# Kernel tuning notes

Hardware: AMD Instinct MI355X
Metric: run time of the kernel (lower is better)

The kernel has to match this reference:

```python
import jax, jax.numpy as jnp
import numpy as np

DIM = 512
GROUPS = 8

def setup_inputs() -> dict:
    key = jax.random.key(0)
    k1, k2, k3, k4, k5 = jax.random.split(key, 5)
    B, L, C = 8, 4096, DIM
    s = 1.0 / np.sqrt(C)
    x = jax.random.normal(k1, (B, L, C), dtype=jnp.float32)
    W_qkv = jax.random.normal(k2, (C, 3 * C), dtype=jnp.float32) * s
    b_qkv = jax.random.normal(k3, (3 * C,), dtype=jnp.float32) * 0.01
    W_proj = jax.random.normal(k4, (C, C), dtype=jnp.float32) * s
    b_proj = jax.random.normal(k5, (C,), dtype=jnp.float32) * 0.01
    return {"x": x, "W_qkv": W_qkv, "b_qkv": b_qkv,
            "W_proj": W_proj, "b_proj": b_proj, "size": 64}

def reference(x, W_qkv, b_qkv, W_proj, b_proj, size):
    B, L, C = x.shape
    g = GROUPS
    hd = C // g  # per-group channel dim
    qkv = x @ W_qkv + b_qkv                       # [B, L, 3C]
    qkv = qkv.reshape(B, L, 3, g, hd).transpose(2, 0, 3, 1, 4)  # [3, B, g, L, hd]
    q, k, v = qkv[0], qkv[1], qkv[2]
    q = q * (float(L) ** -0.5)
    # channel-wise (cross-covariance) attention: [B, g, hd, hd]
    attn = jnp.einsum('bgld,bgle->bgde', q, k)
    attn = jax.nn.softmax(attn, axis=-1)
    out = jnp.einsum('bgde,bgle->bgld', attn, v)  # [B, g, L, hd]
    out = out.transpose(0, 2, 1, 3).reshape(B, L, C)
    out = out @ W_proj + b_proj
    return (out, size)
```

## Files before the change

kernel.cpp:

```cpp
#include <hip/hip_runtime.h>
#include <hip/hip_bf16.h>
#include <stdint.h>

typedef __hip_bfloat16 bf16;
typedef __attribute__((ext_vector_type(8))) short s16x8;
typedef __attribute__((ext_vector_type(4))) float f32x4;

__device__ __forceinline__ short f2bf_bits(float f) {
    union { bf16 b; short s; } u; u.b = __float2bfloat16(f); return u.s;
}

__device__ __forceinline__ void gload_lds16(const void* g, void* l) {
    __builtin_amdgcn_global_load_lds(
        (const __attribute__((address_space(1))) void*)(uintptr_t)g,
        (__attribute__((address_space(3))) void*)(uintptr_t)l,
        16, 0, 0);
}

__device__ __forceinline__ f32x4 mfma16(s16x8 a, s16x8 b, f32x4 c) {
    return __builtin_amdgcn_mfma_f32_16x16x32_bf16(a, b, c, 0, 0, 0);
}

__global__ __launch_bounds__(256) void cvt_bf16_kernel(const float* __restrict__ in,
                                                       bf16* __restrict__ out, int n8) {
    int i = blockIdx.x * blockDim.x + threadIdx.x;
    int stride = gridDim.x * blockDim.x;
    for (; i < n8; i += stride) {
        f32x4 a = ((const f32x4*)in)[2 * i];
        f32x4 b = ((const f32x4*)in)[2 * i + 1];
        s16x8 o;
        o[0] = f2bf_bits(a[0]); o[1] = f2bf_bits(a[1]);
        o[2] = f2bf_bits(a[2]); o[3] = f2bf_bits(a[3]);
        o[4] = f2bf_bits(b[0]); o[5] = f2bf_bits(b[1]);
        o[6] = f2bf_bits(b[2]); o[7] = f2bf_bits(b[3]);
        ((s16x8*)out)[i] = o;
    }
}

__global__ __launch_bounds__(256) void transpose_cvt_kernel(const float* __restrict__ in,
                                                            bf16* __restrict__ out,
                                                            int R, int C) {
    __shared__ float t[32][33];
    int c0 = blockIdx.x * 32, r0 = blockIdx.y * 32;
    int lx = threadIdx.x & 31, ly = threadIdx.x >> 5;
    for (int i = ly; i < 32; i += 8)
        t[i][lx] = in[(size_t)(r0 + i) * C + (c0 + lx)];
    __syncthreads();
    for (int i = ly; i < 32; i += 8)
        out[(size_t)(c0 + i) * R + (r0 + lx)] = __float2bfloat16(t[lx][i]);
}

__global__ __launch_bounds__(256, 2) void gemm_qkv_kernel(
    const bf16* __restrict__ A, const bf16* __restrict__ Bt,
    const float* __restrict__ bias,
    bf16* __restrict__ qT, bf16* __restrict__ kT, bf16* __restrict__ V) {
    __shared__ __align__(16) char smem[33280];
    bf16* As = (bf16*)smem;
    bf16* Bs = (bf16*)(smem + 16384);
    const int tid = threadIdx.x;
    const int wid = tid >> 6, lane = tid & 63;
    const int r16 = lane & 15, rg = lane >> 4;
    const int wr = wid >> 1, wc = wid & 1;
    const int n0 = blockIdx.x * 128;
    const int m0 = blockIdx.y * 128;

    f32x4 acc[4][4] = {};
    for (int ks = 0; ks < 8; ++ks) {
        const int k0 = ks * 64;
#pragma unroll
        for (int it = 0; it < 4; ++it) {
            int f = (it * 256 + tid) << 4;
            int row = f >> 7;
            int sc = ((f >> 4) & 7) ^ (row & 7);
            gload_lds16((const char*)(A + (size_t)(m0 + row) * 512 + k0) + (sc << 4),
                        (char*)As + ((it * 256 + (wid << 6)) << 4));
            gload_lds16((const char*)(Bt + (size_t)(n0 + row) * 512 + k0) + (sc << 4),
                        (char*)Bs + ((it * 256 + (wid << 6)) << 4));
        }
        __syncthreads();
#pragma unroll
        for (int kk = 0; kk < 2; ++kk) {
            s16x8 af[4], bfv[4];
#pragma unroll
            for (int mi = 0; mi < 4; ++mi) {
                int row = (wr << 6) + (mi << 4) + r16;
                int off = (row << 7) + ((((kk << 2) + rg) ^ (row & 7)) << 4);
                af[mi] = *(const s16x8*)((const char*)As + off);
            }
#pragma unroll
            for (int ni = 0; ni < 4; ++ni) {
                int row = (wc << 6) + (ni << 4) + r16;
                int off = (row << 7) + ((((kk << 2) + rg) ^ (row & 7)) << 4);
                bfv[ni] = *(const s16x8*)((const char*)Bs + off);
            }
#pragma unroll
            for (int mi = 0; mi < 4; ++mi)
#pragma unroll
                for (int ni = 0; ni < 4; ++ni)
                    acc[mi][ni] = mfma16(af[mi], bfv[ni], acc[mi][ni]);
        }
        __syncthreads();
    }

    const int bb = m0 >> 12;
    const int l0 = m0 & 4095;
    const float scale = (n0 < 512) ? 0.015625f : 1.0f;
    bf16* tr = (bf16*)smem;
    float bv[4];
#pragma unroll
    for (int ni = 0; ni < 4; ++ni)
        bv[ni] = bias[n0 + (wc << 6) + (ni << 4) + r16];
#pragma unroll
    for (int mi = 0; mi < 4; ++mi)
#pragma unroll
        for (int ni = 0; ni < 4; ++ni) {
            int col = (wc << 6) + (ni << 4) + r16;
#pragma unroll
            for (int r = 0; r < 4; ++r) {
                int row = (wr << 6) + (mi << 4) + (rg << 2) + r;
                tr[row * 130 + col] = __float2bfloat16((acc[mi][ni][r] + bv[ni]) * scale);
            }
        }
    __syncthreads();
    if (n0 < 1024) {
        bf16* dst; int c0;
        if (n0 < 512) { dst = qT; c0 = n0; } else { dst = kT; c0 = n0 - 512; }
#pragma unroll 4
        for (int it = 0; it < 64; ++it) {
            int flat = it * 256 + tid;
            int cl = flat >> 7, ll = flat & 127;
            dst[((size_t)(bb * 512 + c0 + cl) << 12) + (l0 + ll)] = tr[ll * 130 + cl];
        }
    } else {
        int c0 = n0 - 1024;
#pragma unroll 4
        for (int it = 0; it < 64; ++it) {
            int flat = it * 256 + tid;
            int rr = flat >> 7, cc = flat & 127;
            V[((size_t)(m0 + rr) << 9) + (c0 + cc)] = tr[rr * 130 + cc];
        }
    }
}

__global__ __launch_bounds__(256, 2) void s_partial_kernel(
    const bf16* __restrict__ qT, const bf16* __restrict__ kT,
    float* __restrict__ S_part) {
    __shared__ __align__(16) bf16 qs[64 * 64];
    __shared__ __align__(16) bf16 ks2[64 * 64];
    const int chunk = blockIdx.x, bg = blockIdx.y;
    const int tid = threadIdx.x, wid = tid >> 6, lane = tid & 63;
    const int r16 = lane & 15, rg = lane >> 4;
    const int wr = wid >> 1, wc = wid & 1;
    const size_t base = ((size_t)bg << 18) + chunk * 512;
    const bf16* qb = qT + base;
    const bf16* kb = kT + base;
    f32x4 acc[2][2] = {};
    for (int ks = 0; ks < 8; ++ks) {
#pragma unroll
        for (int it = 0; it < 2; ++it) {
            int f = (it * 256 + tid) << 4;
            int row = f >> 7;
            int sc = ((f >> 4) & 7) ^ (row & 7);
            gload_lds16((const char*)(qb + ((size_t)row << 12) + ks * 64) + (sc << 4),
                        (char*)qs + ((it * 256 + (wid << 6)) << 4));
            gload_lds16((const char*)(kb + ((size_t)row << 12) + ks * 64) + (sc << 4),
                        (char*)ks2 + ((it * 256 + (wid << 6)) << 4));
        }
        __syncthreads();
#pragma unroll
        for (int kk = 0; kk < 2; ++kk) {
            s16x8 aq[2], bk[2];
#pragma unroll
            for (int mi = 0; mi < 2; ++mi) {
                int row = (wr << 5) + (mi << 4) + r16;
                int off = (row << 7) + ((((kk << 2) + rg) ^ (row & 7)) << 4);
                aq[mi] = *(const s16x8*)((const char*)qs + off);
            }
#pragma unroll
            for (int ni = 0; ni < 2; ++ni) {
                int row = (wc << 5) + (ni << 4) + r16;
                int off = (row << 7) + ((((kk << 2) + rg) ^ (row & 7)) << 4);
                bk[ni] = *(const s16x8*)((const char*)ks2 + off);
            }
#pragma unroll
            for (int mi = 0; mi < 2; ++mi)
#pragma unroll
                for (int ni = 0; ni < 2; ++ni)
                    acc[mi][ni] = mfma16(aq[mi], bk[ni], acc[mi][ni]);
        }
        __syncthreads();
    }
    float* o = S_part + (((size_t)chunk << 6) + bg) * 4096;
#pragma unroll
    for (int mi = 0; mi < 2; ++mi)
#pragma unroll
        for (int ni = 0; ni < 2; ++ni)
#pragma unroll
            for (int r = 0; r < 4; ++r) {
                int row = (wr << 5) + (mi << 4) + (rg << 2) + r;
                int col = (wc << 5) + (ni << 4) + r16;
                o[(row << 6) + col] = acc[mi][ni][r];
            }
}

__global__ __launch_bounds__(256) void softmax_kernel(const float* __restrict__ S_part,
                                                      bf16* __restrict__ attn) {
    const int bg = blockIdx.x, tid = threadIdx.x;
    const int d = tid >> 2, q = tid & 3;
    const float* base = S_part + ((size_t)bg << 12) + (d << 6) + (q << 4);
    float s[16];
#pragma unroll
    for (int j = 0; j < 16; ++j) s[j] = 0.f;
    for (int p = 0; p < 8; ++p) {
        const float* pp = base + ((size_t)p << 18);
#pragma unroll
        for (int j = 0; j < 16; ++j) s[j] += pp[j];
    }
    float m = s[0];
#pragma unroll
    for (int j = 1; j < 16; ++j) m = fmaxf(m, s[j]);
    m = fmaxf(m, __shfl_xor(m, 1));
    m = fmaxf(m, __shfl_xor(m, 2));
    float sum = 0.f;
#pragma unroll
    for (int j = 0; j < 16; ++j) { s[j] = __expf(s[j] - m); sum += s[j]; }
    sum += __shfl_xor(sum, 1);
    sum += __shfl_xor(sum, 2);
    float inv = 1.0f / sum;
    bf16* o = attn + ((size_t)bg << 12) + (d << 6) + (q << 4);
#pragma unroll
    for (int j = 0; j < 16; ++j) o[j] = __float2bfloat16(s[j] * inv);
}

__global__ __launch_bounds__(256, 2) void pv_kernel(const bf16* __restrict__ V,
                                                    const bf16* __restrict__ attn,
                                                    bf16* __restrict__ aout) {
    const int lc = blockIdx.x, bg = blockIdx.y;
    const int b = bg >> 3, g = bg & 7;
    const int tid = threadIdx.x, wid = tid >> 6, lane = tid & 63;
    const int r16 = lane & 15, rg = lane >> 4;
    const bf16* ab = attn + ((size_t)bg << 12);
    s16x8 bfr[4][2];
#pragma unroll
    for (int ni = 0; ni < 4; ++ni)
#pragma unroll
        for (int kk = 0; kk < 2; ++kk)
            bfr[ni][kk] = *(const s16x8*)(ab + (((ni << 4) + r16) << 6) + (kk << 5) + (rg << 3));
    const size_t mrow = (size_t)b * 4096 + lc * 256 + wid * 64;
    const bf16* vb = V + (mrow << 9) + (g << 6);
    f32x4 acc[4][4] = {};
#pragma unroll
    for (int mi = 0; mi < 4; ++mi) {
#pragma unroll
        for (int kk = 0; kk < 2; ++kk) {
            s16x8 af = *(const s16x8*)(vb + (((size_t)(mi << 4) + r16) << 9) + (kk << 5) + (rg << 3));
#pragma unroll
            for (int ni = 0; ni < 4; ++ni)
                acc[mi][ni] = mfma16(af, bfr[ni][kk], acc[mi][ni]);
        }
    }
    bf16* ob = aout + (mrow << 9) + (g << 6);
#pragma unroll
    for (int mi = 0; mi < 4; ++mi)
#pragma unroll
        for (int ni = 0; ni < 4; ++ni)
#pragma unroll
            for (int r = 0; r < 4; ++r)
                ob[((size_t)((mi << 4) + (rg << 2) + r) << 9) + (ni << 4) + r16] =
                    __float2bfloat16(acc[mi][ni][r]);
}

__global__ __launch_bounds__(256, 2) void gemm_proj_kernel(
    const bf16* __restrict__ A, const bf16* __restrict__ Bt,
    const float* __restrict__ bias, float* __restrict__ out) {
    __shared__ __align__(16) char smem[32768];
    bf16* As = (bf16*)smem;
    bf16* Bs = (bf16*)(smem + 16384);
    const int tid = threadIdx.x;
    const int wid = tid >> 6, lane = tid & 63;
    const int r16 = lane & 15, rg = lane >> 4;
    const int wr = wid >> 1, wc = wid & 1;
    const int n0 = blockIdx.x * 128;
    const int m0 = blockIdx.y * 128;
    f32x4 acc[4][4] = {};
    for (int ks = 0; ks < 8; ++ks) {
        const int k0 = ks * 64;
#pragma unroll
        for (int it = 0; it < 4; ++it) {
            int f = (it * 256 + tid) << 4;
            int row = f >> 7;
            int sc = ((f >> 4) & 7) ^ (row & 7);
            gload_lds16((const char*)(A + (size_t)(m0 + row) * 512 + k0) + (sc << 4),
                        (char*)As + ((it * 256 + (wid << 6)) << 4));
            gload_lds16((const char*)(Bt + (size_t)(n0 + row) * 512 + k0) + (sc << 4),
                        (char*)Bs + ((it * 256 + (wid << 6)) << 4));
        }
        __syncthreads();
#pragma unroll
        for (int kk = 0; kk < 2; ++kk) {
            s16x8 af[4], bfv[4];
#pragma unroll
            for (int mi = 0; mi < 4; ++mi) {
                int row = (wr << 6) + (mi << 4) + r16;
                int off = (row << 7) + ((((kk << 2) + rg) ^ (row & 7)) << 4);
                af[mi] = *(const s16x8*)((const char*)As + off);
            }
#pragma unroll
            for (int ni = 0; ni < 4; ++ni) {
                int row = (wc << 6) + (ni << 4) + r16;
                int off = (row << 7) + ((((kk << 2) + rg) ^ (row & 7)) << 4);
                bfv[ni] = *(const s16x8*)((const char*)Bs + off);
            }
#pragma unroll
            for (int mi = 0; mi < 4; ++mi)
#pragma unroll
                for (int ni = 0; ni < 4; ++ni)
                    acc[mi][ni] = mfma16(af[mi], bfv[ni], acc[mi][ni]);
        }
        __syncthreads();
    }
    float bv[4];
#pragma unroll
    for (int ni = 0; ni < 4; ++ni)
        bv[ni] = bias[n0 + (wc << 6) + (ni << 4) + r16];
#pragma unroll
    for (int mi = 0; mi < 4; ++mi)
#pragma unroll
        for (int ni = 0; ni < 4; ++ni)
#pragma unroll
            for (int r = 0; r < 4; ++r)
                out[(size_t)(m0 + (wr << 6) + (mi << 4) + (rg << 2) + r) * 512 +
                    (n0 + (wc << 6) + (ni << 4) + r16)] = acc[mi][ni][r] + bv[ni];
}

__global__ void tail_kernel(const int* __restrict__ sz, float* __restrict__ out) {
    out[0] = (float)sz[0];
}

extern "C" void kernel_launch(void* const* d_in, const int* in_sizes, int n_in,
                              void* d_out, int out_size, void* d_ws, size_t ws_size,
                              hipStream_t stream) {
    const float* x      = (const float*)d_in[0];
    const float* W_qkv  = (const float*)d_in[1];
    const float* b_qkv  = (const float*)d_in[2];
    const float* W_proj = (const float*)d_in[3];
    const float* b_proj = (const float*)d_in[4];
    const int*   size_p = (const int*)d_in[5];
    float* out = (float*)d_out;

    char* ws = (char*)d_ws;
    bf16* xb      = (bf16*)ws;
    bf16* Wqkv_t  = (bf16*)(ws + 33554432);
    bf16* Wproj_t = (bf16*)(ws + 35127296);
    bf16* qT      = (bf16*)(ws + 35651584);
    bf16* kT      = (bf16*)(ws + 69206016);
    bf16* V       = (bf16*)(ws + 102760448);
    float* S_part = (float*)xb;
    bf16*  attn   = (bf16*)(ws + 8388608);
    bf16*  aout   = qT;

    cvt_bf16_kernel<<<dim3(2048), dim3(256), 0, stream>>>(x, xb, 2097152);
    transpose_cvt_kernel<<<dim3(48, 16), dim3(256), 0, stream>>>(W_qkv, Wqkv_t, 512, 1536);
    transpose_cvt_kernel<<<dim3(16, 16), dim3(256), 0, stream>>>(W_proj, Wproj_t, 512, 512);
    gemm_qkv_kernel<<<dim3(12, 256), dim3(256), 0, stream>>>(xb, Wqkv_t, b_qkv, qT, kT, V);
    s_partial_kernel<<<dim3(8, 64), dim3(256), 0, stream>>>(qT, kT, S_part);
    softmax_kernel<<<dim3(64), dim3(256), 0, stream>>>(S_part, attn);
    pv_kernel<<<dim3(16, 64), dim3(256), 0, stream>>>(V, attn, aout);
    gemm_proj_kernel<<<dim3(4, 256), dim3(256), 0, stream>>>(aout, Wproj_t, b_proj, out);
    tail_kernel<<<1, 1, 0, stream>>>(size_p, out + (out_size - 1));
    (void)in_sizes; (void)n_in; (void)ws_size;
}
```

Before: 264.8 us.

## Remap GEMM block order for XCD locality and split attention-score reduction finer

Both GEMM kernels remap the flat block index so consecutive blocks are spread across the 8 XCDs in contiguous runs, with the aim of improving L2 reuse of A and B tiles. The score-partial kernel now uses 16 L-chunks of 256 instead of 8 of 512, doubling the block count so more CUs are busy. The softmax is reworked to match: it runs as 4x64 blocks, each thread reduces 4 columns over 16 partials with vector loads, and stores packed bf16. The attn buffer is moved to a later offset because the larger S_part now overlaps the old location.

```diff
diff --git a/kernel.cpp b/kernel.cpp
--- a/kernel.cpp
+++ b/kernel.cpp
@@ -4,6 +4,7 @@
 
 typedef __hip_bfloat16 bf16;
 typedef __attribute__((ext_vector_type(8))) short s16x8;
+typedef __attribute__((ext_vector_type(4))) short s16x4;
 typedef __attribute__((ext_vector_type(4))) float f32x4;
 
 __device__ __forceinline__ short f2bf_bits(float f) {
@@ -61,8 +62,10 @@
     const int wid = tid >> 6, lane = tid & 63;
     const int r16 = lane & 15, rg = lane >> 4;
     const int wr = wid >> 1, wc = wid & 1;
-    const int n0 = blockIdx.x * 128;
-    const int m0 = blockIdx.y * 128;
+    const int flat = blockIdx.y * 12 + blockIdx.x;
+    const int nb = (flat & 7) * 384 + (flat >> 3);
+    const int n0 = (nb % 12) * 128;
+    const int m0 = (nb / 12) * 128;
 
     f32x4 acc[4][4] = {};
     for (int ks = 0; ks < 8; ++ks) {
@@ -127,16 +130,16 @@
         if (n0 < 512) { dst = qT; c0 = n0; } else { dst = kT; c0 = n0 - 512; }
 #pragma unroll 4
         for (int it = 0; it < 64; ++it) {
-            int flat = it * 256 + tid;
-            int cl = flat >> 7, ll = flat & 127;
+            int flat2 = it * 256 + tid;
+            int cl = flat2 >> 7, ll = flat2 & 127;
             dst[((size_t)(bb * 512 + c0 + cl) << 12) + (l0 + ll)] = tr[ll * 130 + cl];
         }
     } else {
         int c0 = n0 - 1024;
 #pragma unroll 4
         for (int it = 0; it < 64; ++it) {
-            int flat = it * 256 + tid;
-            int rr = flat >> 7, cc = flat & 127;
+            int flat2 = it * 256 + tid;
+            int rr = flat2 >> 7, cc = flat2 & 127;
             V[((size_t)(m0 + rr) << 9) + (c0 + cc)] = tr[rr * 130 + cc];
         }
     }
@@ -151,11 +154,11 @@
     const int tid = threadIdx.x, wid = tid >> 6, lane = tid & 63;
     const int r16 = lane & 15, rg = lane >> 4;
     const int wr = wid >> 1, wc = wid & 1;
-    const size_t base = ((size_t)bg << 18) + chunk * 512;
+    const size_t base = ((size_t)bg << 18) + chunk * 256;
     const bf16* qb = qT + base;
     const bf16* kb = kT + base;
     f32x4 acc[2][2] = {};
-    for (int ks = 0; ks < 8; ++ks) {
+    for (int ks = 0; ks < 4; ++ks) {
 #pragma unroll
         for (int it = 0; it < 2; ++it) {
             int f = (it * 256 + tid) << 4;
@@ -205,31 +208,34 @@
 
 __global__ __launch_bounds__(256) void softmax_kernel(const float* __restrict__ S_part,
                                                       bf16* __restrict__ attn) {
-    const int bg = blockIdx.x, tid = threadIdx.x;
-    const int d = tid >> 2, q = tid & 3;
-    const float* base = S_part + ((size_t)bg << 12) + (d << 6) + (q << 4);
-    float s[16];
-#pragma unroll
-    for (int j = 0; j < 16; ++j) s[j] = 0.f;
-    for (int p = 0; p < 8; ++p) {
-        const float* pp = base + ((size_t)p << 18);
-#pragma unroll
-        for (int j = 0; j < 16; ++j) s[j] += pp[j];
-    }
-    float m = s[0];
-#pragma unroll
-    for (int j = 1; j < 16; ++j) m = fmaxf(m, s[j]);
+    const int q4 = blockIdx.x, bg = blockIdx.y;
+    const int tid = threadIdx.x;
+    const int dl = tid >> 4, es = tid & 15;
+    const int d = (q4 << 4) + dl;
+    const float* base = S_part + ((size_t)bg << 12) + (d << 6) + (es << 2);
+    float s[4] = {0.f, 0.f, 0.f, 0.f};
+#pragma unroll
+    for (int p = 0; p < 16; ++p) {
+        f32x4 v4 = *(const f32x4*)(base + ((size_t)p << 18));
+        s[0] += v4[0]; s[1] += v4[1]; s[2] += v4[2]; s[3] += v4[3];
+    }
+    float m = fmaxf(fmaxf(s[0], s[1]), fmaxf(s[2], s[3]));
     m = fmaxf(m, __shfl_xor(m, 1));
     m = fmaxf(m, __shfl_xor(m, 2));
+    m = fmaxf(m, __shfl_xor(m, 4));
+    m = fmaxf(m, __shfl_xor(m, 8));
     float sum = 0.f;
 #pragma unroll
-    for (int j = 0; j < 16; ++j) { s[j] = __expf(s[j] - m); sum += s[j]; }
+    for (int j = 0; j < 4; ++j) { s[j] = __expf(s[j] - m); sum += s[j]; }
     sum += __shfl_xor(sum, 1);
     sum += __shfl_xor(sum, 2);
+    sum += __shfl_xor(sum, 4);
+    sum += __shfl_xor(sum, 8);
     float inv = 1.0f / sum;
-    bf16* o = attn + ((size_t)bg << 12) + (d << 6) + (q << 4);
-#pragma unroll
-    for (int j = 0; j < 16; ++j) o[j] = __float2bfloat16(s[j] * inv);
+    s16x4 w;
+#pragma unroll
+    for (int j = 0; j < 4; ++j) w[j] = f2bf_bits(s[j] * inv);
+    *(s16x4*)(attn + ((size_t)bg << 12) + (d << 6) + (es << 2)) = w;
 }
 
 __global__ __launch_bounds__(256, 2) void pv_kernel(const bf16* __restrict__ V,
@@ -280,8 +286,10 @@
     const int wid = tid >> 6, lane = tid & 63;
     const int r16 = lane & 15, rg = lane >> 4;
     const int wr = wid >> 1, wc = wid & 1;
-    const int n0 = blockIdx.x * 128;
-    const int m0 = blockIdx.y * 128;
+    const int flat = blockIdx.y * 4 + blockIdx.x;
+    const int nb = (flat & 7) * 128 + (flat >> 3);
+    const int n0 = (nb & 3) * 128;
+    const int m0 = (nb >> 2) * 128;
     f32x4 acc[4][4] = {};
     for (int ks = 0; ks < 8; ++ks) {
         const int k0 = ks * 64;
@@ -356,15 +364,15 @@
     bf16* kT      = (bf16*)(ws + 69206016);
     bf16* V       = (bf16*)(ws + 102760448);
     float* S_part = (float*)xb;
-    bf16*  attn   = (bf16*)(ws + 8388608);
+    bf16*  attn   = (bf16*)(ws + 16777216);
     bf16*  aout   = qT;
 
     cvt_bf16_kernel<<<dim3(2048), dim3(256), 0, stream>>>(x, xb, 2097152);
     transpose_cvt_kernel<<<dim3(48, 16), dim3(256), 0, stream>>>(W_qkv, Wqkv_t, 512, 1536);
     transpose_cvt_kernel<<<dim3(16, 16), dim3(256), 0, stream>>>(W_proj, Wproj_t, 512, 512);
     gemm_qkv_kernel<<<dim3(12, 256), dim3(256), 0, stream>>>(xb, Wqkv_t, b_qkv, qT, kT, V);
-    s_partial_kernel<<<dim3(8, 64), dim3(256), 0, stream>>>(qT, kT, S_part);
-    softmax_kernel<<<dim3(64), dim3(256), 0, stream>>>(S_part, attn);
+    s_partial_kernel<<<dim3(16, 64), dim3(256), 0, stream>>>(qT, kT, S_part);
+    softmax_kernel<<<dim3(4, 64), dim3(256), 0, stream>>>(S_part, attn);
     pv_kernel<<<dim3(16, 64), dim3(256), 0, stream>>>(V, attn, aout);
     gemm_proj_kernel<<<dim3(4, 256), dim3(256), 0, stream>>>(aout, Wproj_t, b_proj, out);
     tail_kernel<<<1, 1, 0, stream>>>(size_p, out + (out_size - 1));
```

After: 260.9 us. No clear change (-1.5%).
